# Optimization experiments

Measured on AMD Instinct MI355X. Metric: run time of the kernel, lower is better.

## Reference

```python
import jax, jax.numpy as jnp
import numpy as np

C_REG = 50.0  # soft-SVM regularization from __init__ default C=50


def kronecker(A, B):
    # torch: einsum('ab,cd->acbd').view(a*c, b*d)
    return jnp.einsum('ab,cd->acbd', A, B).reshape(
        A.shape[0] * B.shape[0], A.shape[1] * B.shape[1])


def setup_inputs() -> dict:
    key = jax.random.key(0)
    k1, k2, k3, k4 = jax.random.split(key, 4)
    N_c, N_S, N_Q, C, W, H = 16, 25, 15, 3, 32, 32
    D_feat = 640
    S_k = jax.random.normal(k1, (N_c, N_S, C, W, H), dtype=jnp.float32)
    Q_k = jax.random.normal(k2, (N_c, N_Q, C, W, H), dtype=jnp.float32)
    # base_net modeled as Flatten -> Linear(C*W*H, D_feat), no bias
    W_base = jax.random.normal(k3, (C * W * H, D_feat), dtype=jnp.float32) * 0.02
    gamma = jax.random.normal(k4, (1,), dtype=jnp.float32)
    return {"S_k": S_k, "Q_k": Q_k, "W_base": W_base, "gamma": gamma}


def reference(S_k, Q_k, W_base, gamma):
    N_c, N_S = S_k.shape[:2]
    N_Q = Q_k.shape[1]
    # base_net: flatten image dims, project to features
    f_x = S_k.reshape(N_c * N_S, -1) @ W_base  # placeholder
    f_x = Q_k.reshape(N_c * N_Q, -1) @ W_base          # [N_c*N_Q, D]
    K = S_k.reshape(N_c * N_S, -1) @ W_base            # [N_c*N_S, D]
    # kernel matrix + ridge
    aul = K @ K.T + C_REG * jnp.eye(N_c * N_S, dtype=K.dtype)  # [N_c*N_S, N_c*N_S]
    # explicit Kronecker expansion to the full (N_c^2*N_S) system
    Q = kronecker(jnp.eye(N_c, dtype=K.dtype), aul)    # [N_c^2*N_S, N_c^2*N_S]
    p = kronecker(jnp.eye(N_c, dtype=K.dtype),
                  jnp.ones((1, N_S), dtype=K.dtype)).reshape(-1, 1)
    alpha = jnp.linalg.solve(Q, jax.lax.stop_gradient(p))  # p is detached in torch
    alpha = alpha.reshape(N_c, -1)                     # [N_c, N_c*N_S]
    w_k = alpha @ K                                    # [N_c, D]
    logits = -gamma * (f_x @ w_k.T)                    # [N_c*N_Q, N_c]
    return logits
```

## Files before the change

### kernel.cpp

```cpp
#include <hip/hip_runtime.h>
#include <math.h>

#define DIN 3072
#define DF 640
#define MROWS 400
#define QROWS 240
#define NMAT 400
#define PN 416
#define NRHS 16
#define CREG 50.0f
#define PVSTEPS 5
#define CSTEPS 25
#define KSPLIT 4
#define GBLK 13
#define SCOLS 32
#define SPAD 40
#define FPAD 72
#define MTILES 28

typedef __attribute__((ext_vector_type(8))) short bf8v;
typedef __attribute__((ext_vector_type(4))) short s4v;
typedef __attribute__((ext_vector_type(4))) float f32x4;

__device__ __forceinline__ short bf16_rn(float x) {
  unsigned u = __float_as_uint(x);
  u += 0x7FFFu + ((u >> 16) & 1u);
  return (short)(u >> 16);
}
__device__ __forceinline__ void split_sh(float x, short& h, short& l) {
  h = bf16_rn(x);
  float hf = __uint_as_float(((unsigned)(unsigned short)h) << 16);
  l = bf16_rn(x - hf);
}
__device__ __forceinline__ float bf2f(short h) {
  return __uint_as_float(((unsigned)(unsigned short)h) << 16);
}

__global__ __launch_bounds__(256) void gemm_feat_sk(const float* __restrict__ S,
                                                    const float* __restrict__ Qm,
                                                    const float* __restrict__ Wb,
                                                    float* __restrict__ Acc) {
  __shared__ short Ash[64][FPAD];
  __shared__ short Asl[64][FPAD];
  __shared__ short Bsh[64][FPAD];
  __shared__ short Bsl[64][FPAD];
  int tid = threadIdx.x;
  int wave = tid >> 6, lane = tid & 63, l16 = lane & 15, quad = lane >> 4;
  int by = blockIdx.y, bx = blockIdx.x, bz = blockIdx.z;
  int colBase = bx * 64;
  int kbeg = bz * (DIN / KSPLIT), kend = kbeg + (DIN / KSPLIT);
  int arow = by * 64 + (tid >> 4);
  const float* sr = (arow < MROWS) ? (S + (size_t)arow * DIN)
                                   : (Qm + (size_t)(arow - MROWS) * DIN);
  int kc4 = (tid & 15) * 4;
  float4 ar4[4], br4[4];
  auto load_regs = [&](int kk) {
#pragma unroll
    for (int p = 0; p < 4; ++p) {
      int rowoff = 16 * p;
      const float* srp;
      {
        int ar_ = by * 64 + (tid >> 4) + rowoff;
        srp = (ar_ < MROWS) ? (S + (size_t)ar_ * DIN) : (Qm + (size_t)(ar_ - MROWS) * DIN);
      }
      ar4[p] = *reinterpret_cast<const float4*>(srp + kk + kc4);
      int r = (tid >> 4) + rowoff;
      br4[p] = *reinterpret_cast<const float4*>(Wb + (size_t)(kk + r) * DF + colBase + kc4);
    }
  };
  auto split_write = [&]() {
#pragma unroll
    for (int p = 0; p < 4; ++p) {
      int row = (tid >> 4) + 16 * p;
      s4v hv, lv; short h, l;
      split_sh(ar4[p].x, h, l); hv[0] = h; lv[0] = l;
      split_sh(ar4[p].y, h, l); hv[1] = h; lv[1] = l;
      split_sh(ar4[p].z, h, l); hv[2] = h; lv[2] = l;
      split_sh(ar4[p].w, h, l); hv[3] = h; lv[3] = l;
      *reinterpret_cast<s4v*>(&Ash[row][kc4]) = hv;
      *reinterpret_cast<s4v*>(&Asl[row][kc4]) = lv;
      split_sh(br4[p].x, h, l); Bsh[kc4 + 0][row] = h; Bsl[kc4 + 0][row] = l;
      split_sh(br4[p].y, h, l); Bsh[kc4 + 1][row] = h; Bsl[kc4 + 1][row] = l;
      split_sh(br4[p].z, h, l); Bsh[kc4 + 2][row] = h; Bsl[kc4 + 2][row] = l;
      split_sh(br4[p].w, h, l); Bsh[kc4 + 3][row] = h; Bsl[kc4 + 3][row] = l;
    }
  };
  f32x4 acc[4] = {{0,0,0,0},{0,0,0,0},{0,0,0,0},{0,0,0,0}};
  load_regs(kbeg);
  split_write();
  __syncthreads();
  int k0 = kbeg;
  while (true) {
    int kn = k0 + 64;
    bool more = (kn < kend);
    if (more) load_regs(kn);
#pragma unroll
    for (int kk = 0; kk < 64; kk += 32) {
      int ko = kk + quad * 8;
      bf8v ah = *reinterpret_cast<const bf8v*>(&Ash[wave * 16 + l16][ko]);
      bf8v al = *reinterpret_cast<const bf8v*>(&Asl[wave * 16 + l16][ko]);
#pragma unroll
      for (int t = 0; t < 4; ++t) {
        bf8v bh = *reinterpret_cast<const bf8v*>(&Bsh[t * 16 + l16][ko]);
        bf8v bl = *reinterpret_cast<const bf8v*>(&Bsl[t * 16 + l16][ko]);
        acc[t] = __builtin_amdgcn_mfma_f32_16x16x32_bf16(ah, bh, acc[t], 0, 0, 0);
        acc[t] = __builtin_amdgcn_mfma_f32_16x16x32_bf16(ah, bl, acc[t], 0, 0, 0);
        acc[t] = __builtin_amdgcn_mfma_f32_16x16x32_bf16(al, bh, acc[t], 0, 0, 0);
      }
    }
    if (!more) break;
    __syncthreads();
    split_write();
    __syncthreads();
    k0 = kn;
  }
  float* Ap = Acc + (size_t)bz * 640 * DF;
  int row0 = by * 64 + wave * 16;
#pragma unroll
  for (int t = 0; t < 4; ++t)
#pragma unroll
    for (int r = 0; r < 4; ++r) {
      int row = row0 + quad * 4 + r;
      int col = colBase + t * 16 + l16;
      Ap[(size_t)row * DF + col] = acc[t][r];
    }
}

__global__ __launch_bounds__(256) void feat_reduce(const float* __restrict__ Acc,
                                                   short* __restrict__ Kh,
                                                   short* __restrict__ Kl,
                                                   float* __restrict__ FX,
                                                   float* __restrict__ zbuf,
                                                   float* __restrict__ out) {
  int tid = threadIdx.x;
  if (blockIdx.x == 0) {
    for (int e = tid; e < 14160; e += 256) zbuf[e] = 0.f;
  } else if (blockIdx.x == 1) {
    for (int e = tid; e < QROWS * NRHS; e += 256) out[e] = 0.f;
  }
  int idx = blockIdx.x * 256 + tid;
  if (idx >= 640 * DF) return;
  float v = Acc[idx] + Acc[idx + 409600] + Acc[idx + 819200] + Acc[idx + 1228800];
  int row = idx / DF, col = idx - row * DF;
  if (row < MROWS) {
    short h, l; split_sh(v, h, l);
    Kh[(size_t)row * DF + col] = h;
    Kl[(size_t)row * DF + col] = l;
  } else {
    FX[(size_t)(row - MROWS) * DF + col] = v;
  }
}

__global__ __launch_bounds__(256) void gemm_aul(const short* __restrict__ Kh,
                                                const short* __restrict__ Kl,
                                                short* __restrict__ Aph,
                                                short* __restrict__ Apl) {
  int tid = threadIdx.x;
  int wave = tid >> 6, lane = tid & 63;
  int l16 = lane & 15, quad = lane >> 4;
  int row0 = blockIdx.y * 64 + wave * 16;
  int colBase = blockIdx.x * 64;
  bool aValid = (row0 < MROWS);
  const bf8v bzero = {0,0,0,0,0,0,0,0};
  f32x4 acc[4] = {{0,0,0,0},{0,0,0,0},{0,0,0,0},{0,0,0,0}};
  for (int k0 = 0; k0 < DF; k0 += 32) {
    int ka = k0 + quad * 8;
    bf8v ah = bzero, al = bzero;
    if (aValid) {
      size_t ao = (size_t)(row0 + l16) * DF + ka;
      ah = *reinterpret_cast<const bf8v*>(Kh + ao);
      al = *reinterpret_cast<const bf8v*>(Kl + ao);
    }
#pragma unroll
    for (int t = 0; t < 4; ++t) {
      int colt = colBase + t * 16;
      bf8v bh = bzero, bl = bzero;
      if (colt < MROWS) {
        size_t bo = (size_t)(colt + l16) * DF + ka;
        bh = *reinterpret_cast<const bf8v*>(Kh + bo);
        bl = *reinterpret_cast<const bf8v*>(Kl + bo);
      }
      acc[t] = __builtin_amdgcn_mfma_f32_16x16x32_bf16(ah, bh, acc[t], 0, 0, 0);
      acc[t] = __builtin_amdgcn_mfma_f32_16x16x32_bf16(ah, bl, acc[t], 0, 0, 0);
      acc[t] = __builtin_amdgcn_mfma_f32_16x16x32_bf16(al, bh, acc[t], 0, 0, 0);
    }
  }
  if (row0 >= PN) return;
#pragma unroll
  for (int t = 0; t < 4; ++t) {
    int colt = colBase + t * 16;
    if (colt >= PN) continue;
#pragma unroll
    for (int r = 0; r < 4; ++r) {
      int row = row0 + quad * 4 + r;
      int col = colt + l16;
      float v = acc[t][r];
      if (row == col && row < MROWS) v += CREG;
      short h, l; split_sh(v, h, l);
      size_t o = (size_t)row * PN + col;
      Aph[o] = h; Apl[o] = l;
    }
  }
}

__global__ __launch_bounds__(256) void solve_and_m(const short* __restrict__ Aph,
                                                   const short* __restrict__ Apl,
                                                   const float* __restrict__ FX,
                                                   const short* __restrict__ Kh,
                                                   const short* __restrict__ Kl,
                                                   const float* __restrict__ gamma,
                                                   float* __restrict__ Y0,
                                                   float* __restrict__ Y1,
                                                   float* __restrict__ V0,
                                                   float* __restrict__ V1,
                                                   float* __restrict__ rq,
                                                   unsigned* __restrict__ bar,
                                                   unsigned* __restrict__ mflag,
                                                   float* __restrict__ M,
                                                   float* __restrict__ out) {
  int tid = threadIdx.x, b = blockIdx.x;
  int wave = tid >> 6, lane = tid & 63, l16 = lane & 15, quad = lane >> 4;
  const bf8v bzero = {0,0,0,0,0,0,0,0};

  if (b >= GBLK) {
    int mt = b - GBLK;
    int mb = mt / 7, nb = mt - (mt / 7) * 7;
    int q0 = mb * 64 + wave * 16;
    f32x4 acc[4] = {{0,0,0,0},{0,0,0,0},{0,0,0,0},{0,0,0,0}};
    int arow = q0 + l16;
    bool aOk = (arow < QROWS);
    const float* fr = FX + (size_t)(aOk ? arow : 0) * DF;
    for (int k0 = 0; k0 < DF; k0 += 32) {
      int ka = k0 + quad * 8;
      bf8v ah = bzero, al = bzero;
      if (aOk) {
        float4 a0 = *reinterpret_cast<const float4*>(fr + ka);
        float4 a1 = *reinterpret_cast<const float4*>(fr + ka + 4);
        float av[8] = {a0.x, a0.y, a0.z, a0.w, a1.x, a1.y, a1.z, a1.w};
#pragma unroll
        for (int j = 0; j < 8; ++j) { short h, l; split_sh(av[j], h, l); ah[j] = h; al[j] = l; }
      }
#pragma unroll
      for (int t = 0; t < 4; ++t) {
        int n = nb * 64 + t * 16 + l16;
        bf8v bh = bzero, bl = bzero;
        if (n < NMAT) {
          bh = *reinterpret_cast<const bf8v*>(Kh + (size_t)n * DF + ka);
          bl = *reinterpret_cast<const bf8v*>(Kl + (size_t)n * DF + ka);
        }
        acc[t] = __builtin_amdgcn_mfma_f32_16x16x32_bf16(ah, bh, acc[t], 0, 0, 0);
        acc[t] = __builtin_amdgcn_mfma_f32_16x16x32_bf16(ah, bl, acc[t], 0, 0, 0);
        acc[t] = __builtin_amdgcn_mfma_f32_16x16x32_bf16(al, bh, acc[t], 0, 0, 0);
      }
    }
#pragma unroll
    for (int t = 0; t < 4; ++t)
#pragma unroll
      for (int r = 0; r < 4; ++r) {
        int row = q0 + quad * 4 + r;
        int col = nb * 64 + t * 16 + l16;
        if (row < QROWS && col < NMAT)
          __hip_atomic_store(&M[(size_t)row * NMAT + col], acc[t][r],
                             __ATOMIC_RELAXED, __HIP_MEMORY_SCOPE_AGENT);
      }
    __syncthreads();
    if (tid == 0)
      __hip_atomic_fetch_add(mflag, 1u, __ATOMIC_RELEASE, __HIP_MEMORY_SCOPE_AGENT);
    return;
  }

  __shared__ __align__(16) short AsT_h[PN][SPAD];
  __shared__ short AsT_l[PN][SPAD];
  __shared__ short dbT_h[16][SPAD];
  __shared__ short dbT_l[16][SPAD];
  __shared__ float pvp[SCOLS], pvc[SCOLS];
  __shared__ float scal[2];
  __shared__ float XsL[SCOLS][NRHS + 1];
  int r0 = b * SCOLS;

  for (int e = tid; e < SCOLS * (PN / 8); e += 256) {
    int jl = e / (PN / 8), ic = e - (e / (PN / 8)) * (PN / 8);
    bf8v vh = *reinterpret_cast<const bf8v*>(Aph + (size_t)(r0 + jl) * PN + ic * 8);
    bf8v vl = *reinterpret_cast<const bf8v*>(Apl + (size_t)(r0 + jl) * PN + ic * 8);
#pragma unroll
    for (int u = 0; u < 8; ++u) {
      AsT_h[ic * 8 + u][jl] = vh[u];
      AsT_l[ic * 8 + u][jl] = vl[u];
    }
  }
  for (int e = tid; e < 16 * SPAD; e += 256) {
    (&dbT_h[0][0])[e] = 0; (&dbT_l[0][0])[e] = 0;
  }
  __syncthreads();
  if (tid < SCOLS) {
    int gi = r0 + tid;
    float v = (gi < NMAT) ? (1.f + 0.125f * (float)(gi & 7)) : 0.f;
    pvc[tid] = v; pvp[tid] = 0.f;
    dbT_h[0][tid] = bf16_rn(v);
  }
  __syncthreads();

  unsigned ph = 0;
  auto gridbar = [&]() {
    __syncthreads();
    ++ph;
    if (tid == 0) {
      unsigned tgt = ph * GBLK;
      __hip_atomic_fetch_add(bar, 1u, __ATOMIC_RELEASE, __HIP_MEMORY_SCOPE_AGENT);
      while (__hip_atomic_load(bar, __ATOMIC_RELAXED, __HIP_MEMORY_SCOPE_AGENT) < tgt)
        __builtin_amdgcn_s_sleep(2);
    }
    __syncthreads();
  };

  for (int s = 0; s < PVSTEPS; ++s) {
    float* Yv = (s & 1) ? V1 : V0;
    for (int t = wave; t < 26; t += 4) {
      f32x4 acc = {0, 0, 0, 0};
      bf8v bh = *reinterpret_cast<const bf8v*>(&dbT_h[l16][quad * 8]);
      bf8v ah = *reinterpret_cast<const bf8v*>(&AsT_h[t * 16 + l16][quad * 8]);
      acc = __builtin_amdgcn_mfma_f32_16x16x32_bf16(ah, bh, acc, 0, 0, 0);
      if (l16 == 0) {
#pragma unroll
        for (int r_ = 0; r_ < 4; ++r_)
          atomicAdd(&Yv[t * 16 + quad * 4 + r_], acc[r_]);
      }
    }
    gridbar();
    if (tid < SCOLS) {
      float y = atomicExch(&Yv[r0 + tid], 0.f);
      float v = y * (1.f / 4096.f);
      pvp[tid] = pvc[tid];
      pvc[tid] = v;
      dbT_h[0][tid] = bf16_rn(v);
    }
    __syncthreads();
  }
  if (tid == 0) {
    float n = 0.f, dd = 0.f;
    for (int u = 0; u < SCOLS; ++u) { n += pvp[u] * pvc[u]; dd += pvp[u] * pvp[u]; }
    atomicAdd(&rq[0], n);
    atomicAdd(&rq[1], dd);
  }
  gridbar();
  if (tid == 0) {
    float rn = atomicAdd(&rq[0], 0.f), rd = atomicAdd(&rq[1], 0.f);
    float rqv = 4096.f * rn / rd;
    float bb = 1.3f * rqv;
    if (!(bb > 800.f)) bb = 12000.f;
    if (bb > 100000.f) bb = 100000.f;
    scal[0] = 0.5f * (bb + CREG);
    scal[1] = 0.5f * (bb - CREG);
  }
  __syncthreads();
  float theta = scal[0], delta = scal[1];
  float sigma = theta / delta, rho = 1.f / sigma;

  float xr[2], rr[2], dr[2];
#pragma unroll
  for (int m = 0; m < 2; ++m) {
    int rl = (tid >> 4) + 16 * m, c = tid & 15, gi = r0 + rl;
    float pc = (gi < NMAT && (gi / 25) == c) ? 1.f : 0.f;
    xr[m] = 0.f; rr[m] = pc; dr[m] = pc / theta;
    short h, l; split_sh(dr[m], h, l);
    dbT_h[c][rl] = h; dbT_l[c][rl] = l;
  }
  __syncthreads();

  for (int k = 0; k < CSTEPS - 1; ++k) {
    float* Yv = (k & 1) ? Y1 : Y0;
    for (int t = wave; t < 26; t += 4) {
      f32x4 acc = {0, 0, 0, 0};
      bf8v bh = *reinterpret_cast<const bf8v*>(&dbT_h[l16][quad * 8]);
      bf8v bl = *reinterpret_cast<const bf8v*>(&dbT_l[l16][quad * 8]);
      bf8v ah = *reinterpret_cast<const bf8v*>(&AsT_h[t * 16 + l16][quad * 8]);
      bf8v al = *reinterpret_cast<const bf8v*>(&AsT_l[t * 16 + l16][quad * 8]);
      acc = __builtin_amdgcn_mfma_f32_16x16x32_bf16(ah, bh, acc, 0, 0, 0);
      acc = __builtin_amdgcn_mfma_f32_16x16x32_bf16(ah, bl, acc, 0, 0, 0);
      acc = __builtin_amdgcn_mfma_f32_16x16x32_bf16(al, bh, acc, 0, 0, 0);
#pragma unroll
      for (int r_ = 0; r_ < 4; ++r_)
        atomicAdd(&Yv[(t * 16 + quad * 4 + r_) * 16 + l16], acc[r_]);
    }
    gridbar();
    float rho1 = 1.f / (2.f * sigma - rho);
    float s1 = rho1 * rho, s2 = 2.f * rho1 / delta;
    rho = rho1;
#pragma unroll
    for (int m = 0; m < 2; ++m) {
      int rl = (tid >> 4) + 16 * m, c = tid & 15, gi = r0 + rl;
      float mv = atomicExch(&Yv[gi * 16 + c], 0.f);
      xr[m] += dr[m];
      rr[m] -= mv;
      float dn = s1 * dr[m] + s2 * rr[m];
      dr[m] = dn;
      short h, l; split_sh(dn, h, l);
      dbT_h[c][rl] = h; dbT_l[c][rl] = l;
    }
    __syncthreads();
  }
#pragma unroll
  for (int m = 0; m < 2; ++m) {
    int rl = (tid >> 4) + 16 * m, c = tid & 15;
    XsL[rl][c] = xr[m] + dr[m];
  }
  __syncthreads();
  if (tid == 0) {
    while (__hip_atomic_load(mflag, __ATOMIC_RELAXED, __HIP_MEMORY_SCOPE_AGENT) < MTILES)
      __builtin_amdgcn_s_sleep(2);
  }
  __syncthreads();
  float* Msl = reinterpret_cast<float*>(&AsT_h[0][0]);
  for (int e = tid; e < QROWS * SCOLS; e += 256) {
    int q = e >> 5, i = e & 31;
    float v = 0.f;
    if (r0 + i < NMAT)
      v = __hip_atomic_load(&M[(size_t)q * NMAT + r0 + i],
                            __ATOMIC_RELAXED, __HIP_MEMORY_SCOPE_AGENT);
    Msl[e] = v;
  }
  __syncthreads();
  float g = -gamma[0];
  int c = tid & 15;
  for (int q = tid >> 4; q < QROWS; q += 16) {
    float s = 0.f;
#pragma unroll
    for (int i = 0; i < SCOLS; ++i) s += Msl[q * SCOLS + i] * XsL[i][c];
    atomicAdd(&out[q * NRHS + c], g * s);
  }
}

extern "C" void kernel_launch(void* const* d_in, const int* in_sizes, int n_in,
                              void* d_out, int out_size, void* d_ws, size_t ws_size,
                              hipStream_t stream) {
  const float* S = (const float*)d_in[0];
  const float* Qm = (const float*)d_in[1];
  const float* Wb = (const float*)d_in[2];
  const float* gamma = (const float*)d_in[3];
  float* out = (float*)d_out;
  char* base = (char*)d_ws;
  short* Kh   = (short*)(base);
  short* Kl   = (short*)(base + 512000);
  float* FX   = (float*)(base + 1024000);
  short* Aph  = (short*)(base + 1638400);
  short* Apl  = (short*)(base + 1984512);
  float* Mm   = (float*)(base + 2330624);
  unsigned* bar = (unsigned*)(base + 2740224);
  float* rq   = (float*)(base + 2740232);
  unsigned* mflag = (unsigned*)(base + 2740240);
  float* zbuf = (float*)(base + 2740224);
  float* Y0   = (float*)(base + 2740288);
  float* Y1   = (float*)(base + 2766912);
  float* V0   = (float*)(base + 2793536);
  float* V1   = (float*)(base + 2795200);
  float* Acc  = (float*)(base + 2796864);

  gemm_feat_sk<<<dim3(10, 10, KSPLIT), 256, 0, stream>>>(S, Qm, Wb, Acc);
  feat_reduce<<<1600, 256, 0, stream>>>(Acc, Kh, Kl, FX, zbuf, out);
  gemm_aul<<<dim3(7, 7), 256, 0, stream>>>(Kh, Kl, Aph, Apl);
  solve_and_m<<<GBLK + MTILES, 256, 0, stream>>>(Aph, Apl, FX, Kh, Kl, gamma,
                                                 Y0, Y1, V0, V1, rq, bar, mflag,
                                                 Mm, out);
}
```

Before: 229.2 us.

## Fuse split-K reduction into feature GEMM and move final product to M-tile blocks

```diff
diff --git a/kernel.cpp b/kernel.cpp
--- a/kernel.cpp
+++ b/kernel.cpp
@@ -17,6 +17,7 @@
 #define SPAD 40
 #define FPAD 72
 #define MTILES 28
+#define QPER 9
 
 typedef __attribute__((ext_vector_type(8))) short bf8v;
 typedef __attribute__((ext_vector_type(4))) short s4v;
@@ -39,32 +40,35 @@
 __global__ __launch_bounds__(256) void gemm_feat_sk(const float* __restrict__ S,
                                                     const float* __restrict__ Qm,
                                                     const float* __restrict__ Wb,
-                                                    float* __restrict__ Acc) {
+                                                    float* __restrict__ Acc,
+                                                    short* __restrict__ Kh,
+                                                    short* __restrict__ Kl,
+                                                    float* __restrict__ FX,
+                                                    unsigned* __restrict__ tcnt,
+                                                    float* __restrict__ zbuf) {
   __shared__ short Ash[64][FPAD];
   __shared__ short Asl[64][FPAD];
   __shared__ short Bsh[64][FPAD];
   __shared__ short Bsl[64][FPAD];
+  __shared__ unsigned lastf;
   int tid = threadIdx.x;
   int wave = tid >> 6, lane = tid & 63, l16 = lane & 15, quad = lane >> 4;
   int by = blockIdx.y, bx = blockIdx.x, bz = blockIdx.z;
   int colBase = bx * 64;
   int kbeg = bz * (DIN / KSPLIT), kend = kbeg + (DIN / KSPLIT);
-  int arow = by * 64 + (tid >> 4);
-  const float* sr = (arow < MROWS) ? (S + (size_t)arow * DIN)
-                                   : (Qm + (size_t)(arow - MROWS) * DIN);
+  if (bx == 0 && by == 0 && bz == 0) {
+    for (int e = tid; e < 14144; e += 256) zbuf[e] = 0.f;
+  }
   int kc4 = (tid & 15) * 4;
   float4 ar4[4], br4[4];
   auto load_regs = [&](int kk) {
 #pragma unroll
     for (int p = 0; p < 4; ++p) {
-      int rowoff = 16 * p;
-      const float* srp;
-      {
-        int ar_ = by * 64 + (tid >> 4) + rowoff;
-        srp = (ar_ < MROWS) ? (S + (size_t)ar_ * DIN) : (Qm + (size_t)(ar_ - MROWS) * DIN);
-      }
+      int ar_ = by * 64 + (tid >> 4) + 16 * p;
+      const float* srp = (ar_ < MROWS) ? (S + (size_t)ar_ * DIN)
+                                       : (Qm + (size_t)(ar_ - MROWS) * DIN);
       ar4[p] = *reinterpret_cast<const float4*>(srp + kk + kc4);
-      int r = (tid >> 4) + rowoff;
+      int r = (tid >> 4) + 16 * p;
       br4[p] = *reinterpret_cast<const float4*>(Wb + (size_t)(kk + r) * DF + colBase + kc4);
     }
   };
@@ -124,30 +128,26 @@
       int col = colBase + t * 16 + l16;
       Ap[(size_t)row * DF + col] = acc[t][r];
     }
-}
-
-__global__ __launch_bounds__(256) void feat_reduce(const float* __restrict__ Acc,
-                                                   short* __restrict__ Kh,
-                                                   short* __restrict__ Kl,
-                                                   float* __restrict__ FX,
-                                                   float* __restrict__ zbuf,
-                                                   float* __restrict__ out) {
-  int tid = threadIdx.x;
-  if (blockIdx.x == 0) {
-    for (int e = tid; e < 14160; e += 256) zbuf[e] = 0.f;
-  } else if (blockIdx.x == 1) {
-    for (int e = tid; e < QROWS * NRHS; e += 256) out[e] = 0.f;
-  }
-  int idx = blockIdx.x * 256 + tid;
-  if (idx >= 640 * DF) return;
-  float v = Acc[idx] + Acc[idx + 409600] + Acc[idx + 819200] + Acc[idx + 1228800];
-  int row = idx / DF, col = idx - row * DF;
-  if (row < MROWS) {
-    short h, l; split_sh(v, h, l);
-    Kh[(size_t)row * DF + col] = h;
-    Kl[(size_t)row * DF + col] = l;
-  } else {
-    FX[(size_t)(row - MROWS) * DF + col] = v;
+  __syncthreads();
+  if (tid == 0) {
+    unsigned ret = __hip_atomic_fetch_add(&tcnt[by * 10 + bx], 1u,
+                                          __ATOMIC_ACQ_REL, __HIP_MEMORY_SCOPE_AGENT);
+    lastf = (ret == KSPLIT - 1) ? 1u : 0u;
+  }
+  __syncthreads();
+  if (lastf) {
+    for (int e = tid; e < 64 * 64; e += 256) {
+      int rl = e >> 6, cl = e & 63;
+      int row = by * 64 + rl, col = colBase + cl;
+      size_t off = (size_t)row * DF + col;
+      float v = Acc[off] + Acc[off + 409600] + Acc[off + 819200] + Acc[off + 1228800];
+      if (row < MROWS) {
+        short h, l; split_sh(v, h, l);
+        Kh[off] = h; Kl[off] = l;
+      } else {
+        FX[(size_t)(row - MROWS) * DF + col] = v;
+      }
+    }
   }
 }
 
@@ -216,7 +216,9 @@
                                                    float* __restrict__ rq,
                                                    unsigned* __restrict__ bar,
                                                    unsigned* __restrict__ mflag,
+                                                   unsigned* __restrict__ sdone,
                                                    float* __restrict__ M,
+                                                   float* __restrict__ X,
                                                    float* __restrict__ out) {
   int tid = threadIdx.x, b = blockIdx.x;
   int wave = tid >> 6, lane = tid & 63, l16 = lane & 15, quad = lane >> 4;
@@ -266,16 +268,43 @@
     __syncthreads();
     if (tid == 0)
       __hip_atomic_fetch_add(mflag, 1u, __ATOMIC_RELEASE, __HIP_MEMORY_SCOPE_AGENT);
+    __shared__ float Xs[NMAT][NRHS];
+    __shared__ float Mq[QPER][NMAT];
+    int lq0 = mt * QPER;
+    int nq = QROWS - lq0; if (nq > QPER) nq = QPER; if (nq < 0) nq = 0;
+    if (tid == 0) {
+      while (__hip_atomic_load(mflag, __ATOMIC_RELAXED, __HIP_MEMORY_SCOPE_AGENT) < MTILES)
+        __builtin_amdgcn_s_sleep(2);
+      while (__hip_atomic_load(sdone, __ATOMIC_RELAXED, __HIP_MEMORY_SCOPE_AGENT) < GBLK)
+        __builtin_amdgcn_s_sleep(2);
+    }
+    __syncthreads();
+    if (nq == 0) return;
+    for (int e = tid; e < NMAT * NRHS; e += 256)
+      Xs[e >> 4][e & 15] = __hip_atomic_load(&X[e], __ATOMIC_RELAXED, __HIP_MEMORY_SCOPE_AGENT);
+    for (int e = tid; e < nq * NMAT; e += 256) {
+      int ql = e / NMAT, i = e - ql * NMAT;
+      Mq[ql][i] = __hip_atomic_load(&M[(size_t)(lq0 + ql) * NMAT + i],
+                                    __ATOMIC_RELAXED, __HIP_MEMORY_SCOPE_AGENT);
+    }
+    __syncthreads();
+    float g = -gamma[0];
+    int c = tid & 15, qi = tid >> 4;
+    if (qi < nq) {
+      float s = 0.f;
+      for (int i = 0; i < NMAT; ++i) s += Mq[qi][i] * Xs[i][c];
+      __hip_atomic_store(&out[(size_t)(lq0 + qi) * NRHS + c], g * s,
+                         __ATOMIC_RELAXED, __HIP_MEMORY_SCOPE_AGENT);
+    }
     return;
   }
 
-  __shared__ __align__(16) short AsT_h[PN][SPAD];
+  __shared__ short AsT_h[PN][SPAD];
   __shared__ short AsT_l[PN][SPAD];
   __shared__ short dbT_h[16][SPAD];
   __shared__ short dbT_l[16][SPAD];
   __shared__ float pvp[SCOLS], pvc[SCOLS];
   __shared__ float scal[2];
-  __shared__ float XsL[SCOLS][NRHS + 1];
   int r0 = b * SCOLS;
 
   for (int e = tid; e < SCOLS * (PN / 8); e += 256) {
@@ -401,33 +430,14 @@
   }
 #pragma unroll
   for (int m = 0; m < 2; ++m) {
-    int rl = (tid >> 4) + 16 * m, c = tid & 15;
-    XsL[rl][c] = xr[m] + dr[m];
-  }
-  __syncthreads();
-  if (tid == 0) {
-    while (__hip_atomic_load(mflag, __ATOMIC_RELAXED, __HIP_MEMORY_SCOPE_AGENT) < MTILES)
-      __builtin_amdgcn_s_sleep(2);
-  }
-  __syncthreads();
-  float* Msl = reinterpret_cast<float*>(&AsT_h[0][0]);
-  for (int e = tid; e < QROWS * SCOLS; e += 256) {
-    int q = e >> 5, i = e & 31;
-    float v = 0.f;
-    if (r0 + i < NMAT)
-      v = __hip_atomic_load(&M[(size_t)q * NMAT + r0 + i],
-                            __ATOMIC_RELAXED, __HIP_MEMORY_SCOPE_AGENT);
-    Msl[e] = v;
-  }
-  __syncthreads();
-  float g = -gamma[0];
-  int c = tid & 15;
-  for (int q = tid >> 4; q < QROWS; q += 16) {
-    float s = 0.f;
-#pragma unroll
-    for (int i = 0; i < SCOLS; ++i) s += Msl[q * SCOLS + i] * XsL[i][c];
-    atomicAdd(&out[q * NRHS + c], g * s);
-  }
+    int rl = (tid >> 4) + 16 * m, c = tid & 15, gi = r0 + rl;
+    if (gi < NMAT)
+      __hip_atomic_store(&X[gi * NRHS + c], xr[m] + dr[m],
+                         __ATOMIC_RELAXED, __HIP_MEMORY_SCOPE_AGENT);
+  }
+  __syncthreads();
+  if (tid == 0)
+    __hip_atomic_fetch_add(sdone, 1u, __ATOMIC_RELEASE, __HIP_MEMORY_SCOPE_AGENT);
 }
 
 extern "C" void kernel_launch(void* const* d_in, const int* in_sizes, int n_in,
@@ -445,20 +455,25 @@
   short* Aph  = (short*)(base + 1638400);
   short* Apl  = (short*)(base + 1984512);
   float* Mm   = (float*)(base + 2330624);
-  unsigned* bar = (unsigned*)(base + 2740224);
-  float* rq   = (float*)(base + 2740232);
-  unsigned* mflag = (unsigned*)(base + 2740240);
-  float* zbuf = (float*)(base + 2740224);
-  float* Y0   = (float*)(base + 2740288);
-  float* Y1   = (float*)(base + 2766912);
-  float* V0   = (float*)(base + 2793536);
-  float* V1   = (float*)(base + 2795200);
-  float* Acc  = (float*)(base + 2796864);
-
-  gemm_feat_sk<<<dim3(10, 10, KSPLIT), 256, 0, stream>>>(S, Qm, Wb, Acc);
-  feat_reduce<<<1600, 256, 0, stream>>>(Acc, Kh, Kl, FX, zbuf, out);
+  float* Xb   = (float*)(base + 2714624);
+  char* ctrl  = base + 2740224;
+  unsigned* bar   = (unsigned*)(ctrl);
+  float*    rq    = (float*)(ctrl + 8);
+  unsigned* mflag = (unsigned*)(ctrl + 16);
+  unsigned* sdone = (unsigned*)(ctrl + 20);
+  unsigned* tcnt  = (unsigned*)(ctrl + 64);
+  float* Y0   = (float*)(base + 2740736);
+  float* Y1   = (float*)(base + 2767360);
+  float* V0   = (float*)(base + 2793984);
+  float* V1   = (float*)(base + 2795648);
+  float* zbuf = Y0;
+  float* Acc  = (float*)(base + 2797312);
+
+  hipMemsetAsync(ctrl, 0, 512, stream);
+  gemm_feat_sk<<<dim3(10, 10, KSPLIT), 256, 0, stream>>>(S, Qm, Wb, Acc,
+                                                         Kh, Kl, FX, tcnt, zbuf);
   gemm_aul<<<dim3(7, 7), 256, 0, stream>>>(Kh, Kl, Aph, Apl);
   solve_and_m<<<GBLK + MTILES, 256, 0, stream>>>(Aph, Apl, FX, Kh, Kl, gamma,
-                                                 Y0, Y1, V0, V1, rq, bar, mflag,
-                                                 Mm, out);
-}
+                                                 Y0, Y1, V0, V1, rq, bar,
+                                                 mflag, sdone, Mm, Xb, out);
+}
```

Result: slower. 274.9 us (+19.9%).

## Replace atomicAdd output reduction with grid barrier and per-block query slices

Applied to the files above, without the earlier changes.

```diff
diff --git a/kernel.cpp b/kernel.cpp
--- a/kernel.cpp
+++ b/kernel.cpp
@@ -17,6 +17,7 @@
 #define SPAD 40
 #define FPAD 72
 #define MTILES 28
+#define QSLICE 19
 
 typedef __attribute__((ext_vector_type(8))) short bf8v;
 typedef __attribute__((ext_vector_type(4))) short s4v;
@@ -49,22 +50,16 @@
   int by = blockIdx.y, bx = blockIdx.x, bz = blockIdx.z;
   int colBase = bx * 64;
   int kbeg = bz * (DIN / KSPLIT), kend = kbeg + (DIN / KSPLIT);
-  int arow = by * 64 + (tid >> 4);
-  const float* sr = (arow < MROWS) ? (S + (size_t)arow * DIN)
-                                   : (Qm + (size_t)(arow - MROWS) * DIN);
   int kc4 = (tid & 15) * 4;
   float4 ar4[4], br4[4];
   auto load_regs = [&](int kk) {
 #pragma unroll
     for (int p = 0; p < 4; ++p) {
-      int rowoff = 16 * p;
-      const float* srp;
-      {
-        int ar_ = by * 64 + (tid >> 4) + rowoff;
-        srp = (ar_ < MROWS) ? (S + (size_t)ar_ * DIN) : (Qm + (size_t)(ar_ - MROWS) * DIN);
-      }
+      int ar_ = by * 64 + (tid >> 4) + 16 * p;
+      const float* srp = (ar_ < MROWS) ? (S + (size_t)ar_ * DIN)
+                                       : (Qm + (size_t)(ar_ - MROWS) * DIN);
       ar4[p] = *reinterpret_cast<const float4*>(srp + kk + kc4);
-      int r = (tid >> 4) + rowoff;
+      int r = (tid >> 4) + 16 * p;
       br4[p] = *reinterpret_cast<const float4*>(Wb + (size_t)(kk + r) * DF + colBase + kc4);
     }
   };
@@ -130,13 +125,10 @@
                                                    short* __restrict__ Kh,
                                                    short* __restrict__ Kl,
                                                    float* __restrict__ FX,
-                                                   float* __restrict__ zbuf,
-                                                   float* __restrict__ out) {
+                                                   float* __restrict__ zbuf) {
   int tid = threadIdx.x;
   if (blockIdx.x == 0) {
     for (int e = tid; e < 14160; e += 256) zbuf[e] = 0.f;
-  } else if (blockIdx.x == 1) {
-    for (int e = tid; e < QROWS * NRHS; e += 256) out[e] = 0.f;
   }
   int idx = blockIdx.x * 256 + tid;
   if (idx >= 640 * DF) return;
@@ -217,6 +209,7 @@
                                                    unsigned* __restrict__ bar,
                                                    unsigned* __restrict__ mflag,
                                                    float* __restrict__ M,
+                                                   float* __restrict__ X,
                                                    float* __restrict__ out) {
   int tid = threadIdx.x, b = blockIdx.x;
   int wave = tid >> 6, lane = tid & 63, l16 = lane & 15, quad = lane >> 4;
@@ -270,12 +263,11 @@
   }
 
   __shared__ __align__(16) short AsT_h[PN][SPAD];
-  __shared__ short AsT_l[PN][SPAD];
+  __shared__ __align__(16) short AsT_l[PN][SPAD];
   __shared__ short dbT_h[16][SPAD];
   __shared__ short dbT_l[16][SPAD];
   __shared__ float pvp[SCOLS], pvc[SCOLS];
   __shared__ float scal[2];
-  __shared__ float XsL[SCOLS][NRHS + 1];
   int r0 = b * SCOLS;
 
   for (int e = tid; e < SCOLS * (PN / 8); e += 256) {
@@ -401,32 +393,35 @@
   }
 #pragma unroll
   for (int m = 0; m < 2; ++m) {
-    int rl = (tid >> 4) + 16 * m, c = tid & 15;
-    XsL[rl][c] = xr[m] + dr[m];
-  }
-  __syncthreads();
+    int rl = (tid >> 4) + 16 * m, c = tid & 15, gi = r0 + rl;
+    if (gi < NMAT)
+      __hip_atomic_store(&X[gi * NRHS + c], xr[m] + dr[m],
+                         __ATOMIC_RELAXED, __HIP_MEMORY_SCOPE_AGENT);
+  }
+  gridbar();
   if (tid == 0) {
     while (__hip_atomic_load(mflag, __ATOMIC_RELAXED, __HIP_MEMORY_SCOPE_AGENT) < MTILES)
       __builtin_amdgcn_s_sleep(2);
   }
   __syncthreads();
-  float* Msl = reinterpret_cast<float*>(&AsT_h[0][0]);
-  for (int e = tid; e < QROWS * SCOLS; e += 256) {
-    int q = e >> 5, i = e & 31;
-    float v = 0.f;
-    if (r0 + i < NMAT)
-      v = __hip_atomic_load(&M[(size_t)q * NMAT + r0 + i],
-                            __ATOMIC_RELAXED, __HIP_MEMORY_SCOPE_AGENT);
-    Msl[e] = v;
+  float* Xs = reinterpret_cast<float*>(&AsT_h[0][0]);
+  float* Mq = reinterpret_cast<float*>(&AsT_l[0][0]);
+  int lq0 = b * QSLICE;
+  int nq = QROWS - lq0; if (nq > QSLICE) nq = QSLICE; if (nq < 0) nq = 0;
+  for (int e = tid; e < NMAT * NRHS; e += 256)
+    Xs[e] = __hip_atomic_load(&X[e], __ATOMIC_RELAXED, __HIP_MEMORY_SCOPE_AGENT);
+  for (int e = tid; e < nq * NMAT; e += 256) {
+    int ql = e / NMAT, i = e - ql * NMAT;
+    Mq[e] = __hip_atomic_load(&M[(size_t)(lq0 + ql) * NMAT + i],
+                              __ATOMIC_RELAXED, __HIP_MEMORY_SCOPE_AGENT);
   }
   __syncthreads();
   float g = -gamma[0];
-  int c = tid & 15;
-  for (int q = tid >> 4; q < QROWS; q += 16) {
+  for (int e = tid; e < nq * NRHS; e += 256) {
+    int qi = e >> 4, c = e & 15;
     float s = 0.f;
-#pragma unroll
-    for (int i = 0; i < SCOLS; ++i) s += Msl[q * SCOLS + i] * XsL[i][c];
-    atomicAdd(&out[q * NRHS + c], g * s);
+    for (int i = 0; i < NMAT; ++i) s += Mq[qi * NMAT + i] * Xs[i * NRHS + c];
+    out[(size_t)(lq0 + qi) * NRHS + c] = g * s;
   }
 }
 
@@ -445,6 +440,7 @@
   short* Aph  = (short*)(base + 1638400);
   short* Apl  = (short*)(base + 1984512);
   float* Mm   = (float*)(base + 2330624);
+  float* Xb   = (float*)(base + 2714624);
   unsigned* bar = (unsigned*)(base + 2740224);
   float* rq   = (float*)(base + 2740232);
   unsigned* mflag = (unsigned*)(base + 2740240);
@@ -456,9 +452,9 @@
   float* Acc  = (float*)(base + 2796864);
 
   gemm_feat_sk<<<dim3(10, 10, KSPLIT), 256, 0, stream>>>(S, Qm, Wb, Acc);
-  feat_reduce<<<1600, 256, 0, stream>>>(Acc, Kh, Kl, FX, zbuf, out);
+  feat_reduce<<<1600, 256, 0, stream>>>(Acc, Kh, Kl, FX, zbuf);
   gemm_aul<<<dim3(7, 7), 256, 0, stream>>>(Kh, Kl, Aph, Apl);
   solve_and_m<<<GBLK + MTILES, 256, 0, stream>>>(Aph, Apl, FX, Kh, Kl, gamma,
-                                                 Y0, Y1, V0, V1, rq, bar, mflag,
-                                                 Mm, out);
-}
+                                                 Y0, Y1, V0, V1, rq, bar,
+                                                 mflag, Mm, Xb, out);
+}
```

Result: slower. 241.5 us (+5.3%).

## Pre-split inputs to bf16 hi/lo and drop split-K feature GEMM

Applied to the files above, without the earlier changes.

```diff
diff --git a/kernel.cpp b/kernel.cpp
--- a/kernel.cpp
+++ b/kernel.cpp
@@ -11,12 +11,12 @@
 #define CREG 50.0f
 #define PVSTEPS 5
 #define CSTEPS 25
-#define KSPLIT 4
 #define GBLK 13
 #define SCOLS 32
 #define SPAD 40
 #define FPAD 72
 #define MTILES 28
+#define QPER 9
 
 typedef __attribute__((ext_vector_type(8))) short bf8v;
 typedef __attribute__((ext_vector_type(4))) short s4v;
@@ -36,73 +36,113 @@
   return __uint_as_float(((unsigned)(unsigned short)h) << 16);
 }
 
-__global__ __launch_bounds__(256) void gemm_feat_sk(const float* __restrict__ S,
-                                                    const float* __restrict__ Qm,
-                                                    const float* __restrict__ Wb,
-                                                    float* __restrict__ Acc) {
-  __shared__ short Ash[64][FPAD];
-  __shared__ short Asl[64][FPAD];
+__global__ __launch_bounds__(256) void presplit(const float* __restrict__ S,
+                                                const float* __restrict__ Qm,
+                                                const float* __restrict__ Wb,
+                                                short* __restrict__ Ainh,
+                                                short* __restrict__ Ainl,
+                                                short* __restrict__ Wth,
+                                                short* __restrict__ Wtl,
+                                                float* __restrict__ zbuf,
+                                                float* __restrict__ outz) {
+  __shared__ float T[64][65];
+  int tid = threadIdx.x, b = blockIdx.x;
+  if (b < 960) {
+    if (b == 0) {
+      for (int e = tid; e < 14160; e += 256) zbuf[e] = 0.f;
+    } else if (b == 1) {
+      for (int e = tid; e < QROWS * NRHS; e += 256) outz[e] = 0.f;
+    }
+    size_t flat = (size_t)b * 2048 + (size_t)tid * 8;
+    const float* src = (flat < (size_t)MROWS * DIN) ? (S + flat)
+                                                    : (Qm + flat - (size_t)MROWS * DIN);
+    float4 v0 = *reinterpret_cast<const float4*>(src);
+    float4 v1 = *reinterpret_cast<const float4*>(src + 4);
+    float av[8] = {v0.x, v0.y, v0.z, v0.w, v1.x, v1.y, v1.z, v1.w};
+    bf8v hv, lv;
+#pragma unroll
+    for (int j = 0; j < 8; ++j) { short h, l; split_sh(av[j], h, l); hv[j] = h; lv[j] = l; }
+    *reinterpret_cast<bf8v*>(Ainh + flat) = hv;
+    *reinterpret_cast<bf8v*>(Ainl + flat) = lv;
+  } else {
+    int w = b - 960;
+    int n0 = (w % 10) * 64;
+    int k0 = (w / 10) * 64;
+    int c = tid & 63, r0_ = tid >> 6;
+#pragma unroll
+    for (int i = 0; i < 16; ++i) {
+      int r = i * 4 + r0_;
+      T[r][c] = Wb[(size_t)(k0 + r) * DF + n0 + c];
+    }
+    __syncthreads();
+#pragma unroll
+    for (int i = 0; i < 16; ++i) {
+      int n = i * 4 + r0_;
+      float x = T[c][n];
+      short h, l; split_sh(x, h, l);
+      size_t o = (size_t)(n0 + n) * DIN + k0 + c;
+      Wth[o] = h; Wtl[o] = l;
+    }
+  }
+}
+
+__global__ __launch_bounds__(256) void gemm_feat(const short* __restrict__ Ainh,
+                                                 const short* __restrict__ Ainl,
+                                                 const short* __restrict__ Wth,
+                                                 const short* __restrict__ Wtl,
+                                                 short* __restrict__ Kh,
+                                                 short* __restrict__ Kl,
+                                                 float* __restrict__ FX) {
+  __shared__ short Ash[32][FPAD];
+  __shared__ short Asl[32][FPAD];
   __shared__ short Bsh[64][FPAD];
   __shared__ short Bsl[64][FPAD];
   int tid = threadIdx.x;
   int wave = tid >> 6, lane = tid & 63, l16 = lane & 15, quad = lane >> 4;
-  int by = blockIdx.y, bx = blockIdx.x, bz = blockIdx.z;
-  int colBase = bx * 64;
-  int kbeg = bz * (DIN / KSPLIT), kend = kbeg + (DIN / KSPLIT);
-  int arow = by * 64 + (tid >> 4);
-  const float* sr = (arow < MROWS) ? (S + (size_t)arow * DIN)
-                                   : (Qm + (size_t)(arow - MROWS) * DIN);
-  int kc4 = (tid & 15) * 4;
-  float4 ar4[4], br4[4];
+  int bx = blockIdx.x, by = blockIdx.y;
+  int arow_l = tid >> 3, kc8 = (tid & 7) * 8;
+  size_t abase = (size_t)(by * 32 + arow_l) * DIN + kc8;
+  int brow0 = tid >> 3;
+  bf8v pa_h, pa_l, pb_h[2], pb_l[2];
   auto load_regs = [&](int kk) {
-#pragma unroll
-    for (int p = 0; p < 4; ++p) {
-      int rowoff = 16 * p;
-      const float* srp;
-      {
-        int ar_ = by * 64 + (tid >> 4) + rowoff;
-        srp = (ar_ < MROWS) ? (S + (size_t)ar_ * DIN) : (Qm + (size_t)(ar_ - MROWS) * DIN);
-      }
-      ar4[p] = *reinterpret_cast<const float4*>(srp + kk + kc4);
-      int r = (tid >> 4) + rowoff;
-      br4[p] = *reinterpret_cast<const float4*>(Wb + (size_t)(kk + r) * DF + colBase + kc4);
+    pa_h = *reinterpret_cast<const bf8v*>(Ainh + abase + kk);
+    pa_l = *reinterpret_cast<const bf8v*>(Ainl + abase + kk);
+#pragma unroll
+    for (int p = 0; p < 2; ++p) {
+      size_t bb = (size_t)(bx * 64 + brow0 + 32 * p) * DIN + kk + kc8;
+      pb_h[p] = *reinterpret_cast<const bf8v*>(Wth + bb);
+      pb_l[p] = *reinterpret_cast<const bf8v*>(Wtl + bb);
     }
   };
-  auto split_write = [&]() {
-#pragma unroll
-    for (int p = 0; p < 4; ++p) {
-      int row = (tid >> 4) + 16 * p;
-      s4v hv, lv; short h, l;
-      split_sh(ar4[p].x, h, l); hv[0] = h; lv[0] = l;
-      split_sh(ar4[p].y, h, l); hv[1] = h; lv[1] = l;
-      split_sh(ar4[p].z, h, l); hv[2] = h; lv[2] = l;
-      split_sh(ar4[p].w, h, l); hv[3] = h; lv[3] = l;
-      *reinterpret_cast<s4v*>(&Ash[row][kc4]) = hv;
-      *reinterpret_cast<s4v*>(&Asl[row][kc4]) = lv;
-      split_sh(br4[p].x, h, l); Bsh[kc4 + 0][row] = h; Bsl[kc4 + 0][row] = l;
-      split_sh(br4[p].y, h, l); Bsh[kc4 + 1][row] = h; Bsl[kc4 + 1][row] = l;
-      split_sh(br4[p].z, h, l); Bsh[kc4 + 2][row] = h; Bsl[kc4 + 2][row] = l;
-      split_sh(br4[p].w, h, l); Bsh[kc4 + 3][row] = h; Bsl[kc4 + 3][row] = l;
+  auto write_lds = [&]() {
+    *reinterpret_cast<bf8v*>(&Ash[arow_l][kc8]) = pa_h;
+    *reinterpret_cast<bf8v*>(&Asl[arow_l][kc8]) = pa_l;
+#pragma unroll
+    for (int p = 0; p < 2; ++p) {
+      *reinterpret_cast<bf8v*>(&Bsh[brow0 + 32 * p][kc8]) = pb_h[p];
+      *reinterpret_cast<bf8v*>(&Bsl[brow0 + 32 * p][kc8]) = pb_l[p];
     }
   };
-  f32x4 acc[4] = {{0,0,0,0},{0,0,0,0},{0,0,0,0},{0,0,0,0}};
-  load_regs(kbeg);
-  split_write();
-  __syncthreads();
-  int k0 = kbeg;
+  f32x4 acc[2] = {{0,0,0,0},{0,0,0,0}};
+  load_regs(0);
+  write_lds();
+  __syncthreads();
+  int rbase = (wave & 1) * 16 + l16;
+  int cbase = (wave >> 1) * 32;
+  int k0 = 0;
   while (true) {
     int kn = k0 + 64;
-    bool more = (kn < kend);
+    bool more = (kn < DIN);
     if (more) load_regs(kn);
 #pragma unroll
     for (int kk = 0; kk < 64; kk += 32) {
       int ko = kk + quad * 8;
-      bf8v ah = *reinterpret_cast<const bf8v*>(&Ash[wave * 16 + l16][ko]);
-      bf8v al = *reinterpret_cast<const bf8v*>(&Asl[wave * 16 + l16][ko]);
-#pragma unroll
-      for (int t = 0; t < 4; ++t) {
-        bf8v bh = *reinterpret_cast<const bf8v*>(&Bsh[t * 16 + l16][ko]);
-        bf8v bl = *reinterpret_cast<const bf8v*>(&Bsl[t * 16 + l16][ko]);
+      bf8v ah = *reinterpret_cast<const bf8v*>(&Ash[rbase][ko]);
+      bf8v al = *reinterpret_cast<const bf8v*>(&Asl[rbase][ko]);
+#pragma unroll
+      for (int t = 0; t < 2; ++t) {
+        bf8v bh = *reinterpret_cast<const bf8v*>(&Bsh[cbase + t * 16 + l16][ko]);
+        bf8v bl = *reinterpret_cast<const bf8v*>(&Bsl[cbase + t * 16 + l16][ko]);
         acc[t] = __builtin_amdgcn_mfma_f32_16x16x32_bf16(ah, bh, acc[t], 0, 0, 0);
         acc[t] = __builtin_amdgcn_mfma_f32_16x16x32_bf16(ah, bl, acc[t], 0, 0, 0);
         acc[t] = __builtin_amdgcn_mfma_f32_16x16x32_bf16(al, bh, acc[t], 0, 0, 0);
@@ -110,45 +150,25 @@
     }
     if (!more) break;
     __syncthreads();
-    split_write();
+    write_lds();
     __syncthreads();
     k0 = kn;
   }
-  float* Ap = Acc + (size_t)bz * 640 * DF;
-  int row0 = by * 64 + wave * 16;
-#pragma unroll
-  for (int t = 0; t < 4; ++t)
+#pragma unroll
+  for (int t = 0; t < 2; ++t)
 #pragma unroll
     for (int r = 0; r < 4; ++r) {
-      int row = row0 + quad * 4 + r;
-      int col = colBase + t * 16 + l16;
-      Ap[(size_t)row * DF + col] = acc[t][r];
-    }
-}
-
-__global__ __launch_bounds__(256) void feat_reduce(const float* __restrict__ Acc,
-                                                   short* __restrict__ Kh,
-                                                   short* __restrict__ Kl,
-                                                   float* __restrict__ FX,
-                                                   float* __restrict__ zbuf,
-                                                   float* __restrict__ out) {
-  int tid = threadIdx.x;
-  if (blockIdx.x == 0) {
-    for (int e = tid; e < 14160; e += 256) zbuf[e] = 0.f;
-  } else if (blockIdx.x == 1) {
-    for (int e = tid; e < QROWS * NRHS; e += 256) out[e] = 0.f;
-  }
-  int idx = blockIdx.x * 256 + tid;
-  if (idx >= 640 * DF) return;
-  float v = Acc[idx] + Acc[idx + 409600] + Acc[idx + 819200] + Acc[idx + 1228800];
-  int row = idx / DF, col = idx - row * DF;
-  if (row < MROWS) {
-    short h, l; split_sh(v, h, l);
-    Kh[(size_t)row * DF + col] = h;
-    Kl[(size_t)row * DF + col] = l;
-  } else {
-    FX[(size_t)(row - MROWS) * DF + col] = v;
-  }
+      int row = by * 32 + (wave & 1) * 16 + quad * 4 + r;
+      int col = bx * 64 + cbase + t * 16 + l16;
+      float v = acc[t][r];
+      if (row < MROWS) {
+        short h, l; split_sh(v, h, l);
+        Kh[(size_t)row * DF + col] = h;
+        Kl[(size_t)row * DF + col] = l;
+      } else {
+        FX[(size_t)(row - MROWS) * DF + col] = v;
+      }
+    }
 }
 
 __global__ __launch_bounds__(256) void gemm_aul(const short* __restrict__ Kh,
@@ -442,23 +462,28 @@
   short* Kh   = (short*)(base);
   short* Kl   = (short*)(base + 512000);
   float* FX   = (float*)(base + 1024000);
-  short* Aph  = (short*)(base + 1638400);
-  short* Apl  = (short*)(base + 1984512);
-  float* Mm   = (float*)(base + 2330624);
-  unsigned* bar = (unsigned*)(base + 2740224);
-  float* rq   = (float*)(base + 2740232);
-  unsigned* mflag = (unsigned*)(base + 2740240);
-  float* zbuf = (float*)(base + 2740224);
-  float* Y0   = (float*)(base + 2740288);
-  float* Y1   = (float*)(base + 2766912);
-  float* V0   = (float*)(base + 2793536);
-  float* V1   = (float*)(base + 2795200);
-  float* Acc  = (float*)(base + 2796864);
-
-  gemm_feat_sk<<<dim3(10, 10, KSPLIT), 256, 0, stream>>>(S, Qm, Wb, Acc);
-  feat_reduce<<<1600, 256, 0, stream>>>(Acc, Kh, Kl, FX, zbuf, out);
+  float* Xb   = (float*)(base + 1638400);
+  unsigned* bar = (unsigned*)(base + 1664000);
+  float*    rq  = (float*)(base + 1664008);
+  unsigned* mflag = (unsigned*)(base + 1664016);
+  float* zbuf = (float*)(base + 1664000);
+  float* Y0   = (float*)(base + 1664064);
+  float* Y1   = (float*)(base + 1690688);
+  float* V0   = (float*)(base + 1717312);
+  float* V1   = (float*)(base + 1718976);
+  short* Ainh = (short*)(base + 1720640);
+  short* Aph  = (short*)(base + 1720640);
+  short* Apl  = (short*)(base + 2066752);
+  float* Mm   = (float*)(base + 2412864);
+  short* Ainl = (short*)(base + 5652800);
+  short* Wth  = (short*)(base + 9584960);
+  short* Wtl  = (short*)(base + 13517120);
+
+  (void)Xb; (void)ws_size; (void)in_sizes; (void)n_in; (void)out_size;
+  presplit<<<1440, 256, 0, stream>>>(S, Qm, Wb, Ainh, Ainl, Wth, Wtl, zbuf, out);
+  gemm_feat<<<dim3(10, 20), 256, 0, stream>>>(Ainh, Ainl, Wth, Wtl, Kh, Kl, FX);
   gemm_aul<<<dim3(7, 7), 256, 0, stream>>>(Kh, Kl, Aph, Apl);
   solve_and_m<<<GBLK + MTILES, 256, 0, stream>>>(Aph, Apl, FX, Kh, Kl, gamma,
-                                                 Y0, Y1, V0, V1, rq, bar, mflag,
-                                                 Mm, out);
-}
+                                                 Y0, Y1, V0, V1, rq, bar,
+                                                 mflag, Mm, out);
+}
```

After: 233.4 us. About the same (+1.8%).
